# Kernel tuning notes

Measured on AMD Instinct MI355X. Metric: run time of the kernel, lower is better.

## Reference

```python
import jax, jax.numpy as jnp
import numpy as np
from jax import lax

KH = KW = 3
PAD = 1
GROUPS = 3


def setup_inputs() -> dict:
    key = jax.random.key(0)
    k1, k2 = jax.random.split(key)
    x = jax.random.normal(k1, (16, 3, 1024, 1024), dtype=jnp.float32)
    weight = jax.random.normal(k2, (3, 1, KH, KW), dtype=jnp.float32)
    return {"x": x, "weight": weight}


def _norm_conv(x, weight):
    # Normalize each output-channel filter by its L2 norm over the 3x3 window
    w_norm = weight / jnp.linalg.norm(weight.reshape(3, KH * KW), axis=-1).reshape(3, 1, 1, 1)
    xp = jnp.pad(x, ((0, 0), (0, 0), (PAD, PAD), (PAD, PAD)))
    dn = ("NCHW", "OIHW", "NCHW")
    # numerator: depthwise correlation of x with normalized weights
    # (x_patch / ||x_patch||) . w_norm == (x_patch . w_norm) / ||x_patch||
    num = lax.conv_general_dilated(xp, w_norm, (1, 1), "VALID",
                                   dimension_numbers=dn,
                                   feature_group_count=GROUPS)
    ones = jnp.ones((3, 1, KH, KW), x.dtype)
    sq = lax.conv_general_dilated(xp * xp, ones, (1, 1), "VALID",
                                  dimension_numbers=dn,
                                  feature_group_count=GROUPS)
    patch_norm = jnp.sqrt(sq)  # per-(n,c) L2 norm of each 3x3 patch
    return num / patch_norm


def reference(x, weight):
    return _norm_conv(x, weight)
```

## Files before the change

kernel.cpp:

```cpp
#include <hip/hip_runtime.h>


#define HH 1024
#define WW 1024
#define CC 3
#define NN 16
#define ROWS 8
#define TILES (HH / ROWS)
#define NBLK (NN * CC * TILES)

__device__ __forceinline__ void load_row(const float* __restrict__ base, int y,
                                         int x0, float* __restrict__ dst)
{
    if ((unsigned)y >= (unsigned)HH) {
#pragma unroll
        for (int k = 0; k < 6; ++k) dst[k] = 0.f;
    } else {
        const float* p = base + y * WW;
        const float4 c4 = *(const float4*)(p + x0);
        dst[0] = (x0 > 0)      ? p[x0 - 1] : 0.f;
        dst[1] = c4.x; dst[2] = c4.y; dst[3] = c4.z; dst[4] = c4.w;
        dst[5] = (x0 + 4 < WW) ? p[x0 + 4] : 0.f;
    }
}

__global__ __launch_bounds__(256) void normconv_kernel(
    const float* __restrict__ x, const float* __restrict__ w, float* __restrict__ out)
{
    const int b     = blockIdx.x;
    const int L     = (b & 7) * (NBLK / 8) + (b >> 3);
    const int tile  = L & (TILES - 1);
    const int plane = L >> 7;
    const int c     = plane % CC;

    float wn[9];
    float s = 0.f;
#pragma unroll
    for (int i = 0; i < 9; ++i) { float wi = w[c * 9 + i]; wn[i] = wi; s += wi * wi; }
    const float winv = rsqrtf(s);
#pragma unroll
    for (int i = 0; i < 9; ++i) wn[i] *= winv;

    const int x0 = threadIdx.x << 2;
    const int y0 = tile * ROWS;
    const float* base  = x   + (size_t)plane * (HH * WW);
    float*       obase = out + (size_t)plane * (HH * WW);

    float v[3][6];
    load_row(base, y0 - 1, x0, v[0]);
    load_row(base, y0,     x0, v[1]);

#pragma unroll
    for (int i = 0; i < ROWS; ++i) {
        const int y = y0 + i;
        load_row(base, y + 1, x0, v[(i + 2) % 3]);
        const float* r0 = v[(i + 0) % 3];
        const float* r1 = v[(i + 1) % 3];
        const float* r2 = v[(i + 2) % 3];

        float4 o;
        float* op = &o.x;
#pragma unroll
        for (int j = 0; j < 4; ++j) {
            float num = 0.f, sq = 0.f;
#pragma unroll
            for (int k = 0; k < 3; ++k) {
                const float a0 = r0[j + k], a1 = r1[j + k], a2 = r2[j + k];
                num += a0 * wn[k] + a1 * wn[3 + k] + a2 * wn[6 + k];
                sq  += a0 * a0 + a1 * a1 + a2 * a2;
            }
            op[j] = num * rsqrtf(sq);
        }
        *(float4*)(obase + (size_t)y * WW + x0) = o;
    }
}

extern "C" void kernel_launch(void* const* d_in, const int* in_sizes, int n_in,
                              void* d_out, int out_size, void* d_ws, size_t ws_size,
                              hipStream_t stream) {
    const float* x = (const float*)d_in[0];
    const float* w = (const float*)d_in[1];
    float* out = (float*)d_out;

    normconv_kernel<<<NBLK, 256, 0, stream>>>(x, w, out);
}
```

Before: 345.1 us.

## Deepen row prefetch ring, reuse column squares, use nontemporal stores

Doubles rows per block and keeps a 7-slot register ring so each thread issues loads four rows ahead, increasing memory-level parallelism. Column sums of squares are computed once per row and shared across the four outputs, and output writes use nontemporal stores to avoid cache pollution. A min-blocks launch bound is added to cap register use; the deeper ring raises register pressure and halves the number of blocks.

```diff
diff --git a/kernel.cpp b/kernel.cpp
--- a/kernel.cpp
+++ b/kernel.cpp
@@ -5,9 +5,12 @@
 #define WW 1024
 #define CC 3
 #define NN 16
-#define ROWS 8
+#define ROWS 16
 #define TILES (HH / ROWS)
 #define NBLK (NN * CC * TILES)
+#define SLOTS 7
+
+typedef float f32x4 __attribute__((ext_vector_type(4)));
 
 __device__ __forceinline__ void load_row(const float* __restrict__ base, int y,
                                          int x0, float* __restrict__ dst)
@@ -24,13 +27,13 @@
     }
 }
 
-__global__ __launch_bounds__(256) void normconv_kernel(
+__global__ __launch_bounds__(256, 5) void normconv_kernel(
     const float* __restrict__ x, const float* __restrict__ w, float* __restrict__ out)
 {
     const int b     = blockIdx.x;
     const int L     = (b & 7) * (NBLK / 8) + (b >> 3);
     const int tile  = L & (TILES - 1);
-    const int plane = L >> 7;
+    const int plane = L / TILES;
     const int c     = plane % CC;
 
     float wn[9];
@@ -46,32 +49,36 @@
     const float* base  = x   + (size_t)plane * (HH * WW);
     float*       obase = out + (size_t)plane * (HH * WW);
 
-    float v[3][6];
-    load_row(base, y0 - 1, x0, v[0]);
-    load_row(base, y0,     x0, v[1]);
+    float v[SLOTS][6];
+#pragma unroll
+    for (int r = -1; r <= 4; ++r)
+        load_row(base, y0 + r, x0, v[r + 1]);
 
 #pragma unroll
     for (int i = 0; i < ROWS; ++i) {
-        const int y = y0 + i;
-        load_row(base, y + 1, x0, v[(i + 2) % 3]);
-        const float* r0 = v[(i + 0) % 3];
-        const float* r1 = v[(i + 1) % 3];
-        const float* r2 = v[(i + 2) % 3];
+        if (i + 5 <= ROWS)
+            load_row(base, y0 + i + 5, x0, v[(i + 6) % SLOTS]);
 
-        float4 o;
-        float* op = &o.x;
+        const float* r0 = v[(i + 0) % SLOTS];
+        const float* r1 = v[(i + 1) % SLOTS];
+        const float* r2 = v[(i + 2) % SLOTS];
+
+        float colsq[6];
+#pragma unroll
+        for (int t = 0; t < 6; ++t)
+            colsq[t] = r0[t] * r0[t] + r1[t] * r1[t] + r2[t] * r2[t];
+
+        f32x4 o;
 #pragma unroll
         for (int j = 0; j < 4; ++j) {
-            float num = 0.f, sq = 0.f;
+            float num = 0.f;
 #pragma unroll
-            for (int k = 0; k < 3; ++k) {
-                const float a0 = r0[j + k], a1 = r1[j + k], a2 = r2[j + k];
-                num += a0 * wn[k] + a1 * wn[3 + k] + a2 * wn[6 + k];
-                sq  += a0 * a0 + a1 * a1 + a2 * a2;
-            }
-            op[j] = num * rsqrtf(sq);
+            for (int k = 0; k < 3; ++k)
+                num += r0[j + k] * wn[k] + r1[j + k] * wn[3 + k] + r2[j + k] * wn[6 + k];
+            const float sq = colsq[j] + colsq[j + 1] + colsq[j + 2];
+            o[j] = num * rsqrtf(sq);
         }
-        *(float4*)(obase + (size_t)y * WW + x0) = o;
+        __builtin_nontemporal_store(o, (f32x4*)(obase + (size_t)(y0 + i) * WW + x0));
     }
 }
 
```

Result: slower. 559.6 us (+62.1%).
